# Kernel tuning notes

Measured on AMD Instinct MI355X. Metric: run time of the kernel, lower is better.

The kernel has to match this reference:

```python
import jax, jax.numpy as jnp
import numpy as np

Q = 128


def _maxpool2(x):
    # 2x2 max pool, stride 2, NCHW
    return jax.lax.reduce_window(x, -jnp.inf, jax.lax.max,
                                 (1, 1, 2, 2), (1, 1, 2, 2), 'VALID')


def _conv(x, w, b):
    y = jax.lax.conv_general_dilated(x, w, window_strides=(1, 1), padding='VALID',
                                     dimension_numbers=('NCHW', 'OIHW', 'NCHW'))
    return y + b[None, :, None, None]


def setup_inputs() -> dict:
    key = jax.random.key(0)
    ks = jax.random.split(key, 16)
    B = 4096
    x = jax.random.normal(ks[0], (B, 1, 28, 28), dtype=jnp.float32)
    hash_idx1 = jax.random.randint(ks[1], (25,), 0, Q, dtype=jnp.int32)
    hash_idx2 = jax.random.randint(ks[2], (800,), 0, Q, dtype=jnp.int32)
    hash_idx3 = jax.random.randint(ks[3], (1024,), 0, Q, dtype=jnp.int32)
    # random +/-1 signs
    sgn1 = jnp.sign(jax.random.normal(ks[4], (25,), dtype=jnp.float32))
    sgn2 = jnp.sign(jax.random.normal(ks[5], (800,), dtype=jnp.float32))
    sgn3 = jnp.sign(jax.random.normal(ks[6], (1024,), dtype=jnp.float32))
    # compressed (sketched) parameters: one length-Q vector per output unit
    w1 = jax.random.normal(ks[7], (32, Q), dtype=jnp.float32) * 0.2
    b1 = jax.random.normal(ks[8], (32,), dtype=jnp.float32) * 0.05
    w2 = jax.random.normal(ks[9], (64, Q), dtype=jnp.float32) * 0.05
    b2 = jax.random.normal(ks[10], (64,), dtype=jnp.float32) * 0.05
    w3 = jax.random.normal(ks[11], (512, Q), dtype=jnp.float32) * 0.03
    b3 = jax.random.normal(ks[12], (512,), dtype=jnp.float32) * 0.05
    fc2_w = jax.random.normal(ks[13], (10, 512), dtype=jnp.float32) * 0.04
    fc2_b = jax.random.normal(ks[14], (10,), dtype=jnp.float32) * 0.05
    return {'x': x,
            'hash_idx1': hash_idx1, 'hash_idx2': hash_idx2, 'hash_idx3': hash_idx3,
            'sgn1': sgn1, 'sgn2': sgn2, 'sgn3': sgn3,
            'w1': w1, 'b1': b1, 'w2': w2, 'b2': b2, 'w3': w3, 'b3': b3,
            'fc2_w': fc2_w, 'fc2_b': fc2_b}


def reference(x, hash_idx1, hash_idx2, hash_idx3, sgn1, sgn2, sgn3,
              w1, b1, w2, b2, w3, b3, fc2_w, fc2_b):
    # SketchConv1: reconstruct dense weight via gather + sign flip
    wc1 = (w1[:, hash_idx1] * sgn1[None, :]).reshape(32, 1, 5, 5)
    h = jax.nn.relu(_maxpool2(_conv(x, wc1, b1)))          # (B,32,12,12)
    # SketchConv2
    wc2 = (w2[:, hash_idx2] * sgn2[None, :]).reshape(64, 32, 5, 5)
    h = jax.nn.relu(_maxpool2(_conv(h, wc2, b2)))          # (B,64,4,4)
    h = h.reshape(h.shape[0], -1)                          # (B,1024)
    # SketchLinear
    W3 = w3[:, hash_idx3] * sgn3[None, :]                  # (512,1024)
    h = jax.nn.relu(h @ W3.T + b3)                         # (B,512)
    logits = h @ fc2_w.T + fc2_b                           # (B,10)
    return jax.nn.log_softmax(logits, axis=1)
```

## Files before the change

kernel.cpp:

```cpp
#include <hip/hip_runtime.h>
#include <hip/hip_bf16.h>
#include <math.h>


typedef __attribute__((ext_vector_type(8))) short bf16x8;
typedef __attribute__((ext_vector_type(4))) float f32x4;

static __device__ inline ushort f2bfu(float v) {
    union { __hip_bfloat16 h; ushort u; } cv;
    cv.h = __float2bfloat16(v);
    return cv.u;
}


__global__ __launch_bounds__(256)
void k_reconstruct(const float* __restrict__ w1, const float* __restrict__ w2,
                   const float* __restrict__ w3,
                   const int* __restrict__ hi1, const int* __restrict__ hi2,
                   const int* __restrict__ hi3,
                   const float* __restrict__ s1, const float* __restrict__ s2,
                   const float* __restrict__ s3,
                   __hip_bfloat16* __restrict__ wc1f,
                   __hip_bfloat16* __restrict__ wc1s,
                   __hip_bfloat16* __restrict__ wc2f,
                   __hip_bfloat16* __restrict__ W3f) {
    const int t = blockIdx.x * blockDim.x + threadIdx.x;
    bf16x8 o;
    if (t < 256) {
        const bool shifted = t >= 128;
        const int u = t & 127;
        const int nt = u >> 6, lane = u & 63;
        const int quad = lane >> 4, l15 = lane & 15;
        const int oc = nt * 16 + l15;
        #pragma unroll
        for (int j = 0; j < 8; ++j) {
            int tt = quad * 8 + j;
            int ki = (tt * 43) >> 8;
            int kj = tt - 6 * ki;
            float v = 0.f;
            if (!shifted && ki < 5 && kj < 5) {
                int f = ki * 5 + kj;
                v = w1[oc * 128 + hi1[f]] * s1[f];
            } else if (shifted && ki < 5 && kj >= 1 && kj <= 5) {
                int f = ki * 5 + (kj - 1);
                v = w1[oc * 128 + hi1[f]] * s1[f];
            }
            o[j] = (short)f2bfu(v);
        }
        *(bf16x8*)((ushort*)(shifted ? wc1s : wc1f) + (size_t)u * 8) = o;
    } else if (t < 6656) {
        const int u = t - 256;
        const int l15 = u & 15, quad = (u >> 4) & 3;
        const int ntA = (u >> 6) & 3, tap = u >> 8;
        const int oc = ntA * 16 + l15;
        #pragma unroll
        for (int j = 0; j < 8; ++j) {
            int ic = quad * 8 + j;
            int f = ic * 25 + tap;
            o[j] = (short)f2bfu(w2[oc * 128 + hi2[f]] * s2[f]);
        }
        *(bf16x8*)((ushort*)wc2f + (size_t)u * 8) = o;
    } else if (t < 72192) {
        const int u = t - 6656;
        const int l15 = u & 15, quad = (u >> 4) & 3;
        const int kt = (u >> 6) & 31, ntile = u >> 11;
        const int n = ntile * 16 + l15;
        #pragma unroll
        for (int j = 0; j < 8; ++j) {
            int k = kt * 32 + quad * 8 + j;
            o[j] = (short)f2bfu(w3[n * 128 + hi3[k]] * s3[k]);
        }
        *(bf16x8*)((ushort*)W3f + (size_t)u * 8) = o;
    }
}

__global__ __launch_bounds__(512, 6)
void k_conv(const float* __restrict__ x,
            const __hip_bfloat16* __restrict__ wc1f,
            const __hip_bfloat16* __restrict__ wc1s,
            const __hip_bfloat16* __restrict__ wc2f,
            const float* __restrict__ b1, const float* __restrict__ b2,
            __hip_bfloat16* __restrict__ h2) {
    __shared__ __align__(16) ushort s_xb[4 * 816];
    __shared__ __align__(16) ushort s_h1[16 * 1160];

    const int tid = threadIdx.x;
    const int b0 = blockIdx.x * 4;
    const int wave = tid >> 6, lane = tid & 63;
    const int l15 = lane & 15, quad = lane >> 4;

    {
        const float4* xg = (const float4*)(x + (size_t)b0 * 784);
        for (int i = tid; i < 784; i += 512) {
            float4 v = xg[i];
            int img = i / 196;
            int pos = (i - img * 196) * 4;
            ushort* dst = &s_xb[img * 816 + pos];
            dst[0] = f2bfu(v.x); dst[1] = f2bfu(v.y);
            dst[2] = f2bfu(v.z); dst[3] = f2bfu(v.w);
        }
        if (tid < 128) {
            int img = tid >> 5, k = tid & 31;
            s_xb[img * 816 + 784 + k] = 0;
        }
    }

    bf16x8 bw1[2], bw1s[2];
    float bb1[2];
    #pragma unroll
    for (int nt = 0; nt < 2; ++nt) {
        bw1[nt]  = *(const bf16x8*)((const ushort*)wc1f + (nt * 64 + lane) * 8);
        bw1s[nt] = *(const bf16x8*)((const ushort*)wc1s + (nt * 64 + lane) * 8);
        bb1[nt] = b1[nt * 16 + l15];
    }
    __syncthreads();

    {
        const int img = wave >> 1, half = wave & 1;
        const int sub = l15 & 3;
        const ushort* srcImg = s_xb + img * 816;
        int offr[4];
        #pragma unroll
        for (int r = 0; r < 4; ++r) {
            int t = quad * 8 + 2 * r;
            int row = (t * 43) >> 8;
            int col = t - 6 * row;
            offr[r] = row * 28 + col;
        }
        const int g0 = l15 >> 3, r0 = l15 & 7;
        #pragma unroll
        for (int ii = 0; ii < 18; ++ii) {
            const int i = half * 18 + ii;
            const int pb = 4 * i + (l15 >> 2);
            const int pi = (pb * 171) >> 11;
            const int pj = pb - 12 * pi;
            const int base_e = (2 * pi + (sub >> 1)) * 28 + 2 * pj;
            const ushort* p0 = srcImg + base_e;
            union { bf16x8 v; uint u[4]; } A;
            A.u[0] = *(const uint*)(p0 + offr[0]);
            A.u[1] = *(const uint*)(p0 + offr[1]);
            A.u[2] = *(const uint*)(p0 + offr[2]);
            A.u[3] = *(const uint*)(p0 + offr[3]);
            f32x4 z = {0.f, 0.f, 0.f, 0.f};
            f32x4 ce0 = __builtin_amdgcn_mfma_f32_16x16x32_bf16(A.v, bw1[0],  z, 0, 0, 0);
            f32x4 co0 = __builtin_amdgcn_mfma_f32_16x16x32_bf16(A.v, bw1s[0], z, 0, 0, 0);
            f32x4 ce1 = __builtin_amdgcn_mfma_f32_16x16x32_bf16(A.v, bw1[1],  z, 0, 0, 0);
            f32x4 co1 = __builtin_amdgcn_mfma_f32_16x16x32_bf16(A.v, bw1s[1], z, 0, 0, 0);
            const int pbo = 4 * i + quad;
            float m0 = fmaxf(fmaxf(ce0[0], co0[1]), fmaxf(ce0[2], co0[3]));
            float m1 = fmaxf(fmaxf(ce1[0], co1[1]), fmaxf(ce1[2], co1[3]));
            s_h1[(img * 4 + g0) * 1160 + pbo * 8 + r0]     = f2bfu(fmaxf(m0 + bb1[0], 0.f));
            s_h1[(img * 4 + 2 + g0) * 1160 + pbo * 8 + r0] = f2bfu(fmaxf(m1 + bb1[1], 0.f));
        }
    }
    __syncthreads();

    const int pr = wave >> 1, nh = wave & 1;
    const int sub2 = l15 & 3;
    const int ci2 = 2 * pr + (sub2 >> 1);
    const int cj2 = 2 * (l15 >> 2) + (sub2 & 1);
    const int posBase = (ci2 * 12 + cj2) * 8;

    f32x4 acc[4][2];
    float bb2[2];
    #pragma unroll
    for (int ntl = 0; ntl < 2; ++ntl) {
        bb2[ntl] = b2[(nh * 2 + ntl) * 16 + l15];
        #pragma unroll
        for (int img = 0; img < 4; ++img)
            acc[img][ntl] = (f32x4){0.f, 0.f, 0.f, 0.f};
    }

    #pragma unroll
    for (int tap = 0; tap < 25; ++tap) {
        const int ki = tap / 5, kj = tap % 5;
        const int off = (ki * 12 + kj) * 8;
        bf16x8 a[4];
        #pragma unroll
        for (int img = 0; img < 4; ++img)
            a[img] = *(const bf16x8*)&s_h1[(img * 4 + quad) * 1160 + posBase + off];
        #pragma unroll
        for (int ntl = 0; ntl < 2; ++ntl) {
            bf16x8 bf = *(const bf16x8*)((const ushort*)wc2f +
                          ((tap * 4 + nh * 2 + ntl) * 64 + lane) * 8);
            #pragma unroll
            for (int img = 0; img < 4; ++img)
                acc[img][ntl] = __builtin_amdgcn_mfma_f32_16x16x32_bf16(
                    a[img], bf, acc[img][ntl], 0, 0, 0);
        }
    }

    #pragma unroll
    for (int img = 0; img < 4; ++img)
        #pragma unroll
        for (int ntl = 0; ntl < 2; ++ntl) {
            f32x4 c = acc[img][ntl];
            float m = fmaxf(fmaxf(c[0], c[1]), fmaxf(c[2], c[3]));
            float v = fmaxf(m + bb2[ntl], 0.f);
            h2[(size_t)(b0 + img) * 1024 + ((nh * 2 + ntl) * 16 + l15) * 16 + pr * 4 + quad] =
                __float2bfloat16(v);
        }
}

__global__ __launch_bounds__(1024)
void k_fc(const __hip_bfloat16* __restrict__ A, const __hip_bfloat16* __restrict__ W3f,
          const float* __restrict__ b3, const float* __restrict__ fc2w,
          const float* __restrict__ fc2b, float* __restrict__ out) {
    __shared__ __align__(16) ushort s_A[16 * 1032];
    __shared__ float s_h3[16 * 516];

    const int tid = threadIdx.x;
    const int wave = tid >> 6, lane = tid & 63;
    const int l15 = lane & 15, quad = lane >> 4;
    const int mBase = blockIdx.x * 16;

    {
        const uint4* g = (const uint4*)(A + (size_t)(mBase + wave) * 1024);
        uint4 v0 = g[lane * 2], v1 = g[lane * 2 + 1];
        uint4* d = (uint4*)&s_A[wave * 1032 + lane * 16];
        d[0] = v0; d[1] = v1;
    }
    __syncthreads();

    f32x4 acc[2];
    acc[0] = (f32x4){0.f, 0.f, 0.f, 0.f};
    acc[1] = (f32x4){0.f, 0.f, 0.f, 0.f};

    const ushort* aP = &s_A[l15 * 1032 + quad * 8];
    const ushort* bP0 = (const ushort*)W3f + (((size_t)(wave * 2)     * 32) * 64 + lane) * 8;
    const ushort* bP1 = (const ushort*)W3f + (((size_t)(wave * 2 + 1) * 32) * 64 + lane) * 8;
    #pragma unroll 4
    for (int kt = 0; kt < 32; ++kt) {
        bf16x8 a = *(const bf16x8*)(aP + kt * 32);
        bf16x8 bf0 = *(const bf16x8*)(bP0 + kt * 512);
        bf16x8 bf1 = *(const bf16x8*)(bP1 + kt * 512);
        acc[0] = __builtin_amdgcn_mfma_f32_16x16x32_bf16(a, bf0, acc[0], 0, 0, 0);
        acc[1] = __builtin_amdgcn_mfma_f32_16x16x32_bf16(a, bf1, acc[1], 0, 0, 0);
    }

    #pragma unroll
    for (int ntl = 0; ntl < 2; ++ntl) {
        int col = wave * 32 + ntl * 16 + l15;
        float bb = b3[col];
        #pragma unroll
        for (int r = 0; r < 4; ++r)
            s_h3[(quad * 4 + r) * 516 + col] = fmaxf(acc[ntl][r] + bb, 0.f);
    }
    __syncthreads();

    const float* hrow = &s_h3[wave * 516];
    float4 h0 = *(const float4*)&hrow[lane * 8];
    float4 h1 = *(const float4*)&hrow[lane * 8 + 4];
    float lg[10];
    #pragma unroll
    for (int c = 0; c < 10; ++c) {
        float4 w0 = *(const float4*)&fc2w[c * 512 + lane * 8];
        float4 w1 = *(const float4*)&fc2w[c * 512 + lane * 8 + 4];
        float s = h0.x * w0.x + h0.y * w0.y + h0.z * w0.z + h0.w * w0.w
                + h1.x * w1.x + h1.y * w1.y + h1.z * w1.z + h1.w * w1.w;
        s += __shfl_down(s, 32);
        s += __shfl_down(s, 16);
        s += __shfl_down(s, 8);
        s += __shfl_down(s, 4);
        s += __shfl_down(s, 2);
        s += __shfl_down(s, 1);
        lg[c] = s;
    }
    if (lane == 0) {
        float mx = -1e30f;
        #pragma unroll
        for (int c = 0; c < 10; ++c) { lg[c] += fc2b[c]; mx = fmaxf(mx, lg[c]); }
        float sum = 0.f;
        #pragma unroll
        for (int c = 0; c < 10; ++c) sum += expf(lg[c] - mx);
        float lse = mx + logf(sum);
        #pragma unroll
        for (int c = 0; c < 10; ++c)
            out[(size_t)(mBase + wave) * 10 + c] = lg[c] - lse;
    }
}

extern "C" void kernel_launch(void* const* d_in, const int* in_sizes, int n_in,
                              void* d_out, int out_size, void* d_ws, size_t ws_size,
                              hipStream_t stream) {
    const float* x    = (const float*)d_in[0];
    const int*   hi1  = (const int*)d_in[1];
    const int*   hi2  = (const int*)d_in[2];
    const int*   hi3  = (const int*)d_in[3];
    const float* s1   = (const float*)d_in[4];
    const float* s2   = (const float*)d_in[5];
    const float* s3   = (const float*)d_in[6];
    const float* w1   = (const float*)d_in[7];
    const float* b1   = (const float*)d_in[8];
    const float* w2   = (const float*)d_in[9];
    const float* b2   = (const float*)d_in[10];
    const float* w3   = (const float*)d_in[11];
    const float* b3   = (const float*)d_in[12];
    const float* fc2w = (const float*)d_in[13];
    const float* fc2b = (const float*)d_in[14];
    float* out = (float*)d_out;

    const int B = in_sizes[0] / 784;

    char* ws = (char*)d_ws;
    __hip_bfloat16* wc1f = (__hip_bfloat16*)(ws + 0);
    __hip_bfloat16* wc1s = (__hip_bfloat16*)(ws + 2048);
    __hip_bfloat16* wc2f = (__hip_bfloat16*)(ws + 4096);
    __hip_bfloat16* W3f  = (__hip_bfloat16*)(ws + 106496);
    __hip_bfloat16* h2   = (__hip_bfloat16*)(ws + 1155072);

    k_reconstruct<<<(72192 + 255) / 256, 256, 0, stream>>>(
        w1, w2, w3, hi1, hi2, hi3, s1, s2, s3, wc1f, wc1s, wc2f, W3f);
    k_conv<<<B / 4, 512, 0, stream>>>(x, wc1f, wc1s, wc2f, b1, b2, h2);
    k_fc<<<B / 16, 1024, 0, stream>>>(h2, W3f, b3, fc2w, fc2b, out);
}
```

Measured before the change: 142.8 us.

## Shrink conv LDS footprint and spread weight reconstruction over more threads

k_reconstruct now has four threads build each 8-element bf16 fragment, two elements apiece, so the grid is four times larger and per-thread gather latency is shorter. k_conv stages only two input images in LDS at a time, processing conv1 in two passes with an extra barrier per pass. This halves the input staging buffer and raises the launch-bounds occupancy hint from 6 to 8 blocks per CU. In exchange it adds synchronisation and possible register pressure.

```diff
diff --git a/kernel.cpp b/kernel.cpp
--- a/kernel.cpp
+++ b/kernel.cpp
@@ -25,63 +25,72 @@
                    __hip_bfloat16* __restrict__ wc2f,
                    __hip_bfloat16* __restrict__ W3f) {
     const int t = blockIdx.x * blockDim.x + threadIdx.x;
-    bf16x8 o;
-    if (t < 256) {
-        const bool shifted = t >= 128;
-        const int u = t & 127;
+    const int f = t >> 2;
+    const int j0 = (t & 3) * 2;
+    ushort r0, r1;
+    if (f < 256) {
+        const bool shifted = f >= 128;
+        const int u = f & 127;
         const int nt = u >> 6, lane = u & 63;
         const int quad = lane >> 4, l15 = lane & 15;
         const int oc = nt * 16 + l15;
-        #pragma unroll
-        for (int j = 0; j < 8; ++j) {
-            int tt = quad * 8 + j;
+        ushort rr[2];
+        #pragma unroll
+        for (int jj = 0; jj < 2; ++jj) {
+            int tt = quad * 8 + j0 + jj;
             int ki = (tt * 43) >> 8;
             int kj = tt - 6 * ki;
             float v = 0.f;
             if (!shifted && ki < 5 && kj < 5) {
-                int f = ki * 5 + kj;
-                v = w1[oc * 128 + hi1[f]] * s1[f];
+                int fi = ki * 5 + kj;
+                v = w1[oc * 128 + hi1[fi]] * s1[fi];
             } else if (shifted && ki < 5 && kj >= 1 && kj <= 5) {
-                int f = ki * 5 + (kj - 1);
-                v = w1[oc * 128 + hi1[f]] * s1[f];
+                int fi = ki * 5 + (kj - 1);
+                v = w1[oc * 128 + hi1[fi]] * s1[fi];
             }
-            o[j] = (short)f2bfu(v);
-        }
-        *(bf16x8*)((ushort*)(shifted ? wc1s : wc1f) + (size_t)u * 8) = o;
-    } else if (t < 6656) {
-        const int u = t - 256;
+            rr[jj] = f2bfu(v);
+        }
+        r0 = rr[0]; r1 = rr[1];
+        *(uint*)((ushort*)(shifted ? wc1s : wc1f) + (size_t)u * 8 + j0) =
+            (uint)r0 | ((uint)r1 << 16);
+    } else if (f < 6656) {
+        const int u = f - 256;
         const int l15 = u & 15, quad = (u >> 4) & 3;
         const int ntA = (u >> 6) & 3, tap = u >> 8;
         const int oc = ntA * 16 + l15;
-        #pragma unroll
-        for (int j = 0; j < 8; ++j) {
-            int ic = quad * 8 + j;
-            int f = ic * 25 + tap;
-            o[j] = (short)f2bfu(w2[oc * 128 + hi2[f]] * s2[f]);
-        }
-        *(bf16x8*)((ushort*)wc2f + (size_t)u * 8) = o;
-    } else if (t < 72192) {
-        const int u = t - 6656;
+        ushort rr[2];
+        #pragma unroll
+        for (int jj = 0; jj < 2; ++jj) {
+            int ic = quad * 8 + j0 + jj;
+            int fi = ic * 25 + tap;
+            rr[jj] = f2bfu(w2[oc * 128 + hi2[fi]] * s2[fi]);
+        }
+        r0 = rr[0]; r1 = rr[1];
+        *(uint*)((ushort*)wc2f + (size_t)u * 8 + j0) = (uint)r0 | ((uint)r1 << 16);
+    } else if (f < 72192) {
+        const int u = f - 6656;
         const int l15 = u & 15, quad = (u >> 4) & 3;
         const int kt = (u >> 6) & 31, ntile = u >> 11;
         const int n = ntile * 16 + l15;
-        #pragma unroll
-        for (int j = 0; j < 8; ++j) {
-            int k = kt * 32 + quad * 8 + j;
-            o[j] = (short)f2bfu(w3[n * 128 + hi3[k]] * s3[k]);
-        }
-        *(bf16x8*)((ushort*)W3f + (size_t)u * 8) = o;
-    }
-}
-
-__global__ __launch_bounds__(512, 6)
+        ushort rr[2];
+        #pragma unroll
+        for (int jj = 0; jj < 2; ++jj) {
+            int k = kt * 32 + quad * 8 + j0 + jj;
+            rr[jj] = f2bfu(w3[n * 128 + hi3[k]] * s3[k]);
+        }
+        r0 = rr[0]; r1 = rr[1];
+        *(uint*)((ushort*)W3f + (size_t)u * 8 + j0) = (uint)r0 | ((uint)r1 << 16);
+    }
+}
+
+__global__ __launch_bounds__(512, 8)
 void k_conv(const float* __restrict__ x,
             const __hip_bfloat16* __restrict__ wc1f,
             const __hip_bfloat16* __restrict__ wc1s,
             const __hip_bfloat16* __restrict__ wc2f,
             const float* __restrict__ b1, const float* __restrict__ b2,
             __hip_bfloat16* __restrict__ h2) {
-    __shared__ __align__(16) ushort s_xb[4 * 816];
+    __shared__ __align__(16) ushort s_xb[2 * 816];
     __shared__ __align__(16) ushort s_h1[16 * 1160];
 
     const int tid = threadIdx.x;
@@ -89,22 +98,6 @@
     const int wave = tid >> 6, lane = tid & 63;
     const int l15 = lane & 15, quad = lane >> 4;
 
-    {
-        const float4* xg = (const float4*)(x + (size_t)b0 * 784);
-        for (int i = tid; i < 784; i += 512) {
-            float4 v = xg[i];
-            int img = i / 196;
-            int pos = (i - img * 196) * 4;
-            ushort* dst = &s_xb[img * 816 + pos];
-            dst[0] = f2bfu(v.x); dst[1] = f2bfu(v.y);
-            dst[2] = f2bfu(v.z); dst[3] = f2bfu(v.w);
-        }
-        if (tid < 128) {
-            int img = tid >> 5, k = tid & 31;
-            s_xb[img * 816 + 784 + k] = 0;
-        }
-    }
-
     bf16x8 bw1[2], bw1s[2];
     float bb1[2];
     #pragma unroll
@@ -113,47 +106,65 @@
         bw1s[nt] = *(const bf16x8*)((const ushort*)wc1s + (nt * 64 + lane) * 8);
         bb1[nt] = b1[nt * 16 + l15];
     }
-    __syncthreads();
-
-    {
-        const int img = wave >> 1, half = wave & 1;
-        const int sub = l15 & 3;
-        const ushort* srcImg = s_xb + img * 816;
-        int offr[4];
-        #pragma unroll
-        for (int r = 0; r < 4; ++r) {
-            int t = quad * 8 + 2 * r;
-            int row = (t * 43) >> 8;
-            int col = t - 6 * row;
-            offr[r] = row * 28 + col;
-        }
-        const int g0 = l15 >> 3, r0 = l15 & 7;
-        #pragma unroll
-        for (int ii = 0; ii < 18; ++ii) {
-            const int i = half * 18 + ii;
-            const int pb = 4 * i + (l15 >> 2);
-            const int pi = (pb * 171) >> 11;
-            const int pj = pb - 12 * pi;
-            const int base_e = (2 * pi + (sub >> 1)) * 28 + 2 * pj;
-            const ushort* p0 = srcImg + base_e;
-            union { bf16x8 v; uint u[4]; } A;
-            A.u[0] = *(const uint*)(p0 + offr[0]);
-            A.u[1] = *(const uint*)(p0 + offr[1]);
-            A.u[2] = *(const uint*)(p0 + offr[2]);
-            A.u[3] = *(const uint*)(p0 + offr[3]);
-            f32x4 z = {0.f, 0.f, 0.f, 0.f};
-            f32x4 ce0 = __builtin_amdgcn_mfma_f32_16x16x32_bf16(A.v, bw1[0],  z, 0, 0, 0);
-            f32x4 co0 = __builtin_amdgcn_mfma_f32_16x16x32_bf16(A.v, bw1s[0], z, 0, 0, 0);
-            f32x4 ce1 = __builtin_amdgcn_mfma_f32_16x16x32_bf16(A.v, bw1[1],  z, 0, 0, 0);
-            f32x4 co1 = __builtin_amdgcn_mfma_f32_16x16x32_bf16(A.v, bw1s[1], z, 0, 0, 0);
-            const int pbo = 4 * i + quad;
-            float m0 = fmaxf(fmaxf(ce0[0], co0[1]), fmaxf(ce0[2], co0[3]));
-            float m1 = fmaxf(fmaxf(ce1[0], co1[1]), fmaxf(ce1[2], co1[3]));
-            s_h1[(img * 4 + g0) * 1160 + pbo * 8 + r0]     = f2bfu(fmaxf(m0 + bb1[0], 0.f));
-            s_h1[(img * 4 + 2 + g0) * 1160 + pbo * 8 + r0] = f2bfu(fmaxf(m1 + bb1[1], 0.f));
-        }
-    }
-    __syncthreads();
+
+    const int img2 = wave >> 2, quarter = wave & 3;
+    const int sub = l15 & 3;
+    int offr[4];
+    #pragma unroll
+    for (int r = 0; r < 4; ++r) {
+        int tt = quad * 8 + 2 * r;
+        int row = (tt * 43) >> 8;
+        int col = tt - 6 * row;
+        offr[r] = row * 28 + col;
+    }
+    const int g0 = l15 >> 3, r0 = l15 & 7;
+
+    #pragma unroll
+    for (int p = 0; p < 2; ++p) {
+        {
+            const float4* xg = (const float4*)(x + (size_t)(b0 + p * 2) * 784);
+            if (tid < 392) {
+                float4 v = xg[tid];
+                int im = tid / 196;
+                int pos = (tid - im * 196) * 4;
+                ushort* dst = &s_xb[im * 816 + pos];
+                dst[0] = f2bfu(v.x); dst[1] = f2bfu(v.y);
+                dst[2] = f2bfu(v.z); dst[3] = f2bfu(v.w);
+            }
+            if (tid < 64)
+                s_xb[(tid >> 5) * 816 + 784 + (tid & 31)] = 0;
+        }
+        __syncthreads();
+        {
+            const int img = p * 2 + img2;
+            const ushort* srcImg = s_xb + img2 * 816;
+            #pragma unroll
+            for (int ii = 0; ii < 9; ++ii) {
+                const int i = quarter * 9 + ii;
+                const int pb = 4 * i + (l15 >> 2);
+                const int pi = (pb * 171) >> 11;
+                const int pj = pb - 12 * pi;
+                const int base_e = (2 * pi + (sub >> 1)) * 28 + 2 * pj;
+                const ushort* p0 = srcImg + base_e;
+                union { bf16x8 v; uint u[4]; } A;
+                A.u[0] = *(const uint*)(p0 + offr[0]);
+                A.u[1] = *(const uint*)(p0 + offr[1]);
+                A.u[2] = *(const uint*)(p0 + offr[2]);
+                A.u[3] = *(const uint*)(p0 + offr[3]);
+                f32x4 z = {0.f, 0.f, 0.f, 0.f};
+                f32x4 ce0 = __builtin_amdgcn_mfma_f32_16x16x32_bf16(A.v, bw1[0],  z, 0, 0, 0);
+                f32x4 co0 = __builtin_amdgcn_mfma_f32_16x16x32_bf16(A.v, bw1s[0], z, 0, 0, 0);
+                f32x4 ce1 = __builtin_amdgcn_mfma_f32_16x16x32_bf16(A.v, bw1[1],  z, 0, 0, 0);
+                f32x4 co1 = __builtin_amdgcn_mfma_f32_16x16x32_bf16(A.v, bw1s[1], z, 0, 0, 0);
+                const int pbo = 4 * i + quad;
+                float m0 = fmaxf(fmaxf(ce0[0], co0[1]), fmaxf(ce0[2], co0[3]));
+                float m1 = fmaxf(fmaxf(ce1[0], co1[1]), fmaxf(ce1[2], co1[3]));
+                s_h1[(img * 4 + g0) * 1160 + pbo * 8 + r0]     = f2bfu(fmaxf(m0 + bb1[0], 0.f));
+                s_h1[(img * 4 + 2 + g0) * 1160 + pbo * 8 + r0] = f2bfu(fmaxf(m1 + bb1[1], 0.f));
+            }
+        }
+        __syncthreads();
+    }
 
     const int pr = wave >> 1, nh = wave & 1;
     const int sub2 = l15 & 3;
@@ -309,7 +320,7 @@
     __hip_bfloat16* W3f  = (__hip_bfloat16*)(ws + 106496);
     __hip_bfloat16* h2   = (__hip_bfloat16*)(ws + 1155072);
 
-    k_reconstruct<<<(72192 + 255) / 256, 256, 0, stream>>>(
+    k_reconstruct<<<1128, 256, 0, stream>>>(
         w1, w2, w3, hi1, hi2, hi3, s1, s2, s3, wc1f, wc1s, wc2f, W3f);
     k_conv<<<B / 4, 512, 0, stream>>>(x, wc1f, wc1s, wc2f, b1, b2, h2);
     k_fc<<<B / 16, 1024, 0, stream>>>(h2, W3f, b3, fc2w, fc2b, out);
```

Measured after the change: 173.5 us. 1.22x slower.
